# Kernel tuning notes

Hardware: AMD Instinct MI355X
Metric: run time of the kernel (lower is better)

## Reference

```python
import jax, jax.numpy as jnp
import numpy as np

N_INP = 256
N_OUT = 16
H = 1024
UH = 32  # uni_hidden_unit
BATCH = 16384


def setup_inputs() -> dict:
    key = jax.random.key(0)
    ks = jax.random.split(key, 16)
    s = 0.02
    return {
        "x": jax.random.normal(ks[0], (BATCH, N_INP), dtype=jnp.float32),
        # main MLP: n_inp -> 1024 -> 1024 -> n_out
        "W0": jax.random.normal(ks[1], (N_INP, H), dtype=jnp.float32) * s,
        "b0": jnp.zeros((H,), jnp.float32),
        "W1": jax.random.normal(ks[2], (H, H), dtype=jnp.float32) * s,
        "b1": jnp.zeros((H,), jnp.float32),
        "W2": jax.random.normal(ks[3], (H, N_OUT), dtype=jnp.float32) * s,
        "b2": jnp.zeros((N_OUT,), jnp.float32),
        # stacked per-feature uni MLPs: 1 -> UH -> UH -> n_out, one per feature
        "uw1": jax.random.normal(ks[4], (N_INP, UH), dtype=jnp.float32) * s,
        "ub1": jnp.zeros((N_INP, UH), jnp.float32),
        "uw2": jax.random.normal(ks[5], (N_INP, UH, UH), dtype=jnp.float32) * s,
        "ub2": jnp.zeros((N_INP, UH), jnp.float32),
        "uw3": jax.random.normal(ks[6], (N_INP, UH, N_OUT), dtype=jnp.float32) * s,
        "ub3": jnp.zeros((N_INP, N_OUT), jnp.float32),
    }


def reference(x, W0, b0, W1, b1, W2, b2, uw1, ub1, uw2, ub2, uw3, ub3):
    # main MLP: Linear+ReLU, Linear+ReLU, Linear
    y = jax.nn.relu(x @ W0 + b0)
    y = jax.nn.relu(y @ W1 + b1)
    y = y @ W2 + b2  # [B, n_out]

    # per-feature univariate MLPs, vectorized over the feature axis i
    # input to uni MLP i is x[:, i:i+1]  -> first Linear(1, UH)
    h = jax.nn.relu(x[:, :, None] * uw1[None] + ub1[None])       # [B, I, UH]
    h = jax.nn.relu(jnp.einsum('bif,ifo->bio', h, uw2) + ub2[None])  # [B, I, UH]
    u = jnp.einsum('bif,ifo->bio', h, uw3) + ub3[None]           # [B, I, n_out]
    return y + u.sum(axis=1)
```

## Files before the change

kernel.cpp:

```cpp
#include <hip/hip_runtime.h>

typedef unsigned short u16;
typedef __attribute__((ext_vector_type(4))) float f32x4;
typedef __attribute__((ext_vector_type(4))) int i32x4;
typedef __attribute__((ext_vector_type(8))) __bf16 bf16x8;
typedef __attribute__((ext_vector_type(4))) unsigned short u16x4;

#define BATCH 16384
#define NINP 256
#define HID 1024
#define NOUT 16

__device__ __forceinline__ u16 f2bf(float f) {
  unsigned u = __builtin_bit_cast(unsigned, f);
  u += 0x7FFFu + ((u >> 16) & 1u);
  return (u16)(u >> 16);
}
__device__ __forceinline__ f32x4 mfma_bb(bf16x8 a, bf16x8 b, f32x4 c) {
  return __builtin_amdgcn_mfma_f32_16x16x32_bf16(a, b, c, 0, 0, 0);
}
__device__ __forceinline__ void gload_lds16(const void* g, void* l) {
  __builtin_amdgcn_global_load_lds(
      (const __attribute__((address_space(1))) void*)g,
      (__attribute__((address_space(3))) void*)l, 16, 0, 0);
}

static const size_t OFF_H0    = 0;
static const size_t OFF_PARTU = 0;
static const size_t OFF_XB    = 33554432;
static const size_t OFF_PARTF = 33554432;
static const size_t OFF_W0T   = 67108864;
static const size_t OFF_W1T   = 67633152;
static const size_t OFF_W2T   = 69730304;
static const size_t OFF_UWP   = 69763072;
static const size_t OFF_CB    = 70811648;

__global__ __launch_bounds__(256) void k_prep(
    const float* __restrict__ x,
    const float* __restrict__ W0, const float* __restrict__ W1,
    const float* __restrict__ W2,
    const float* __restrict__ uw1, const float* __restrict__ ub1,
    const float* __restrict__ uw2, const float* __restrict__ ub2,
    const float* __restrict__ uw3, const float* __restrict__ b2,
    const float* __restrict__ ub3,
    u16* __restrict__ xb,
    u16* __restrict__ W0T, u16* __restrict__ W1T, u16* __restrict__ W2T,
    char* __restrict__ uwp, float* __restrict__ cb)
{
  __shared__ float tile[32][33];
  const int bid = blockIdx.x;
  const int tid = threadIdx.x;

  if (bid < 1312) {
    const float* src; u16* dst; int K, N, kb, ob;
    if (bid < 256)       { src = W0; dst = W0T; K = 256;  N = 1024; int t = bid;        kb = (t & 7) * 32;  ob = (t >> 3) * 32; }
    else if (bid < 1280) { src = W1; dst = W1T; K = 1024; N = 1024; int t = bid - 256;  kb = (t & 31) * 32; ob = (t >> 5) * 32; }
    else                 { src = W2; dst = W2T; K = 1024; N = 16;   int t = bid - 1280; kb = t * 32;        ob = 0; }
    const int tx = tid & 31, ty = tid >> 5;
    for (int r = ty; r < 32; r += 8)
      if (ob + tx < N) tile[r][tx] = src[(size_t)(kb + r) * N + ob + tx];
    __syncthreads();
    for (int r = ty; r < 32; r += 8)
      if (ob + r < N) dst[(size_t)(ob + r) * K + kb + tx] = f2bf(tile[tx][r]);
  } else if (bid < 5408) {
    const int idx = ((bid - 1312) * 256 + tid) * 4;
    const float4 v = *(const float4*)&x[idx];
    u16x4 o4 = { f2bf(v.x), f2bf(v.y), f2bf(v.z), f2bf(v.w) };
    *(u16x4*)&xb[idx] = o4;
  } else if (bid < 5664) {
    const int e = ((bid - 5408) * 256 + tid) * 4;
    const float4 v = *(const float4*)&uw2[e];
    const int i = e >> 10, f = (e >> 5) & 31, o = e & 31;
    const float vv[4] = { v.x, v.y, v.z, v.w };
    u16* blob16 = (u16*)(uwp + (size_t)i * 4096);
#pragma unroll
    for (int d = 0; d < 4; ++d) {
      const int oo = o + d;
      const int lane = ((f >> 3) << 4) | (oo & 15);
      blob16[256 + (oo >> 4) * 512 + lane * 8 + (f & 7)] = f2bf(vv[d]);
    }
  } else if (bid < 5792) {
    const int e = ((bid - 5664) * 256 + tid) * 4;
    const float4 v = *(const float4*)&uw3[e];
    const int i = e >> 9, f = (e >> 4) & 31, o2 = e & 15;
    const int s = (f < 16) ? (((f >> 2) << 3) + (f & 3))
                           : ((((f - 16) >> 2) << 3) + 4 + (f & 3));
    const float vv[4] = { v.x, v.y, v.z, v.w };
    u16* blob16 = (u16*)(uwp + (size_t)i * 4096);
#pragma unroll
    for (int d = 0; d < 4; ++d)
      blob16[1280 + ((s >> 3) * 16 + o2 + d) * 8 + (s & 7)] = f2bf(vv[d]);
  } else if (bid < 5816) {
    const int e4 = (bid - 5792) * 256 + tid;
    const int i = e4 / 24, r4 = e4 % 24;
    const float* src = (r4 < 8)  ? &uw1[i * 32 + r4 * 4]
                     : (r4 < 16) ? &ub1[i * 32 + (r4 - 8) * 4]
                                 : &ub2[i * 32 + (r4 - 16) * 4];
    *(float4*)(uwp + (size_t)i * 4096 + r4 * 16) = *(const float4*)src;
  } else {
    __shared__ float red[16][16];
    const int ig = tid >> 4, o = tid & 15;
    float s = 0.f;
#pragma unroll
    for (int k = 0; k < 16; ++k) s += ub3[(ig * 16 + k) * 16 + o];
    red[ig][o] = s;
    __syncthreads();
    if (tid < 16) {
      float t = b2[tid];
#pragma unroll
      for (int k = 0; k < 16; ++k) t += red[k][tid];
      cb[tid] = t;
    }
  }
}

template<int KT, bool FOLD>
__device__ __forceinline__ void gemm_body(
    const u16* __restrict__ A, const u16* __restrict__ BT,
    const float* __restrict__ bias, u16* __restrict__ C,
    const u16* __restrict__ W2Tp, float* __restrict__ pfold, int N)
{
  extern __shared__ __align__(16) char lds[];
  const int tid = threadIdx.x;
  const int lane = tid & 63, wid = tid >> 6;
  const int l15 = lane & 15, g = lane >> 4;
  const int wA = wid >> 2;
  const int wn = wid & 3;
  const int nbn = N >> 8;
  int logical = blockIdx.x;
  { const int nwg = gridDim.x;
    if ((nwg & 7) == 0) { const int q = nwg >> 3; logical = (logical & 7) * q + (logical >> 3); } }
  const int bm = logical / nbn, bn = logical - bm * nbn;
  const size_t rb = (size_t)bm * 256, cb = (size_t)bn * 256;

  const int q7 = l15 & 7;
  const int arow0 = wA * 128 + l15;
  const int brow0 = wn * 64 + l15;

  char* const ldsA = lds;
  char* const ldsB = lds + 65536;

  const u16* Ag = A + rb * KT;
  const u16* Bg = BT + cb * KT;

  bf16x8 w2f[8];
  if constexpr (FOLD) {
#pragma unroll
    for (int c = 0; c < 8; ++c)
      w2f[c] = __builtin_bit_cast(bf16x8,
          *(const i32x4*)&W2Tp[l15 * HID + (int)cb + c * 32 + g * 8]);
  }
  float bv[4];
#pragma unroll
  for (int n = 0; n < 4; ++n) bv[n] = bias[cb + wn * 64 + n * 16 + l15];

  f32x4 acc[8][4] = {};
  const int NT = KT >> 6;

#define STAGE(arr, src, ktE, s) do { \
    const int G_ = (s) * 512 + tid; \
    const int row_ = G_ >> 3; \
    const int c8_ = (G_ & 7) ^ (row_ & 7); \
    gload_lds16(&(src)[(size_t)row_ * KT + (ktE) + c8_ * 8], (arr) + G_ * 16); \
  } while (0)

#define ARD(bp, m, kk) (*(const bf16x8*)((bp) + (((arow0 + (m) * 16) * 8 + (((kk) * 4 + g) ^ q7)) << 4)))
#define BRD(bp, n, kk) (*(const bf16x8*)((bp) + (((brow0 + (n) * 16) * 8 + (((kk) * 4 + g) ^ q7)) << 4)))

#define KTILE(Ab, Bb, An, Bn, kt1, LASTT) do {                                 \
    bf16x8 av[4][2], bv0[2][2], bv1[2][2];                                     \
              \
    if (!(LASTT)) { STAGE(Bn, Bg, kt1, 0); STAGE(Bn, Bg, kt1, 1);              \
                    STAGE(Bn, Bg, kt1, 2); STAGE(Bn, Bg, kt1, 3);              \
                    STAGE(An, Ag, kt1, 0); STAGE(An, Ag, kt1, 2);              \
                    STAGE(An, Ag, kt1, 1); STAGE(An, Ag, kt1, 3); }            \
    _Pragma("unroll")                                                          \
    for (int m = 0; m < 4; ++m) { av[m][0] = ARD(Ab, m, 0); av[m][1] = ARD(Ab, m, 1); } \
    _Pragma("unroll")                                                          \
    for (int n = 0; n < 2; ++n) { bv0[n][0] = BRD(Bb, n, 0); bv0[n][1] = BRD(Bb, n, 1); \
                                  bv1[n][0] = BRD(Bb, n + 2, 0); bv1[n][1] = BRD(Bb, n + 2, 1); } \
    _Pragma("unroll")                                                          \
    for (int m = 0; m < 4; ++m)                                                \
      _Pragma("unroll")                                                        \
      for (int n = 0; n < 2; ++n) {                                            \
        acc[m][n]     = mfma_bb(av[m][0], bv0[n][0], acc[m][n]);               \
        acc[m][n]     = mfma_bb(av[m][1], bv0[n][1], acc[m][n]);               \
        acc[m][n + 2] = mfma_bb(av[m][0], bv1[n][0], acc[m][n + 2]);           \
        acc[m][n + 2] = mfma_bb(av[m][1], bv1[n][1], acc[m][n + 2]);           \
      }                                                                        \
    if (LASTT) { asm volatile("s_waitcnt vmcnt(0)" ::: "memory"); }            \
    else       { asm volatile("s_waitcnt vmcnt(8)" ::: "memory"); }            \
    asm volatile("s_barrier" ::: "memory");                                    \
                                             \
    _Pragma("unroll")                                                          \
    for (int m = 0; m < 4; ++m) { av[m][0] = ARD(Ab, m + 4, 0); av[m][1] = ARD(Ab, m + 4, 1); } \
    _Pragma("unroll")                                                          \
    for (int m = 0; m < 4; ++m)                                                \
      _Pragma("unroll")                                                        \
      for (int n = 0; n < 2; ++n) {                                            \
        acc[m + 4][n]     = mfma_bb(av[m][0], bv0[n][0], acc[m + 4][n]);       \
        acc[m + 4][n]     = mfma_bb(av[m][1], bv0[n][1], acc[m + 4][n]);       \
        acc[m + 4][n + 2] = mfma_bb(av[m][0], bv1[n][0], acc[m + 4][n + 2]);   \
        acc[m + 4][n + 2] = mfma_bb(av[m][1], bv1[n][1], acc[m + 4][n + 2]);   \
      }                                                                        \
    if (!(LASTT)) { asm volatile("s_waitcnt vmcnt(2)" ::: "memory"); }         \
    asm volatile("s_barrier" ::: "memory");                                    \
  } while (0)

  STAGE(ldsB, Bg, 0, 0); STAGE(ldsB, Bg, 0, 1);
  STAGE(ldsB, Bg, 0, 2); STAGE(ldsB, Bg, 0, 3);
  STAGE(ldsA, Ag, 0, 0); STAGE(ldsA, Ag, 0, 2);
  STAGE(ldsA, Ag, 0, 1); STAGE(ldsA, Ag, 0, 3);
  asm volatile("s_waitcnt vmcnt(2)" ::: "memory");
  asm volatile("s_barrier" ::: "memory");

  for (int t = 0; t < NT - 1; ++t) {
    const int b = t & 1;
    KTILE(ldsA + b * 32768, ldsB + b * 32768,
          ldsA + (b ^ 1) * 32768, ldsB + (b ^ 1) * 32768,
          (t + 1) << 6, false);
  }
  {
    const int b = (NT - 1) & 1;
    KTILE(ldsA + b * 32768, ldsB + b * 32768,
          ldsA + (b ^ 1) * 32768, ldsB + (b ^ 1) * 32768, 0, true);
  }
#undef KTILE
#undef STAGE
#undef ARD
#undef BRD

  asm volatile("s_waitcnt vmcnt(0)" ::: "memory");

  {
    char* const ep = lds;
#pragma unroll
    for (int h = 0; h < 2; ++h) {
      __syncthreads();
#pragma unroll
      for (int mloc = 0; mloc < 4; ++mloc)
#pragma unroll
        for (int n = 0; n < 4; ++n) {
          const int col = wn * 64 + n * 16 + l15;
#pragma unroll
          for (int r = 0; r < 4; ++r) {
            const int lrow = wA * 64 + mloc * 16 + g * 4 + r;
            *(u16*)(ep + lrow * 512 + ((col * 2) ^ ((lrow & 7) << 4))) =
                f2bf(fmaxf(acc[h * 4 + mloc][n][r] + bv[n], 0.f));
          }
        }
      __syncthreads();
      if constexpr (!FOLD) {
#pragma unroll
        for (int p = 0; p < 8; ++p) {
          const int ci = p * 512 + tid;
          const int lrow = ci >> 5, c16 = ci & 31;
          const i32x4 v = *(const i32x4*)(ep + lrow * 512 + ((c16 * 16) ^ ((lrow & 7) << 4)));
          const int grow = (int)rb + (lrow >> 6) * 128 + h * 64 + (lrow & 63);
          *(i32x4*)&C[(size_t)grow * N + cb + c16 * 8] = v;
        }
      } else {
        const int lrow = wid * 16 + l15;
        f32x4 accf = {0.f, 0.f, 0.f, 0.f};
#pragma unroll
        for (int c = 0; c < 8; ++c) {
          const bf16x8 afr = *(const bf16x8*)(
              ep + lrow * 512 + ((c * 64 + g * 16) ^ ((lrow & 7) << 4)));
          accf = mfma_bb(afr, w2f[c], accf);
        }
        const int rowb2 = (int)rb + (wid >> 2) * 128 + h * 64 + (wid & 3) * 16;
        float* pf = pfold + ((size_t)bn * BATCH + rowb2) * NOUT;
#pragma unroll
        for (int r = 0; r < 4; ++r)
          pf[(g * 4 + r) * NOUT + l15] = accf[r];
      }
    }
  }
}

__global__ __launch_bounds__(512, 2) void k_g1(
    const u16* __restrict__ A, const u16* __restrict__ BT,
    const float* __restrict__ bias, u16* __restrict__ C, int N)
{
  gemm_body<256, false>(A, BT, bias, C, nullptr, nullptr, N);
}
__global__ __launch_bounds__(512, 2) void k_g2(
    const u16* __restrict__ A, const u16* __restrict__ BT,
    const float* __restrict__ bias, const u16* __restrict__ W2Tp,
    float* __restrict__ pfold, int N)
{
  gemm_body<1024, true>(A, BT, bias, nullptr, W2Tp, pfold, N);
}

__global__ __launch_bounds__(256, 4) void k_uni(
    const float* __restrict__ x,
    const char* __restrict__ uwp,
    float* __restrict__ part)
{
  const int tid = threadIdx.x, lane = tid & 63, wid = tid >> 6;
  const int l15 = lane & 15, g = lane >> 4;
  const int chunk = blockIdx.x & 7, rowblk = blockIdx.x >> 3;
  const int rb_blk = rowblk * 128;
  const int rb = rb_blk + wid * 32;
  const int i0 = chunk * 32;

  __shared__ __align__(16) float xt[128][33];
  __shared__ __align__(16) char wbuf[3][4096];

  {
    const int r0 = tid >> 3, c4 = (tid & 7) << 2;
#pragma unroll
    for (int rr = 0; rr < 128; rr += 32)
      *(float4*)&xt[rr + r0][c4] =
          *(const float4*)&x[(size_t)(rb_blk + rr + r0) * NINP + i0 + c4];
  }
  gload_lds16(uwp + (size_t)i0 * 4096 + tid * 16, &wbuf[0][tid * 16]);
  gload_lds16(uwp + (size_t)(i0 + 1) * 4096 + tid * 16, &wbuf[1][tid * 16]);
  __syncthreads();

  const f32x4 zero4 = {0.f, 0.f, 0.f, 0.f};
  f32x4 acc0 = zero4, acc1 = zero4;
  const float* xr0 = &xt[wid * 32 + l15][0];
  const float* xr1 = &xt[wid * 32 + 16 + l15][0];

#pragma unroll 2
  for (int ii = 0; ii < 32; ++ii) {
    const int nf = i0 + ((ii + 2) & 31);
    gload_lds16(uwp + (size_t)nf * 4096 + tid * 16,
                &wbuf[(ii + 2) % 3][tid * 16]);

    const char* bp = &wbuf[ii % 3][0];
    const f32x4 w1lo = *(const f32x4*)(bp + g * 32);
    const f32x4 w1hi = *(const f32x4*)(bp + g * 32 + 16);
    const f32x4 b1lo = *(const f32x4*)(bp + 128 + g * 32);
    const f32x4 b1hi = *(const f32x4*)(bp + 128 + g * 32 + 16);
    const f32x4 bb0  = *(const f32x4*)(bp + 256 + g * 16);
    const f32x4 bb1  = *(const f32x4*)(bp + 320 + g * 16);
    const bf16x8 bv0 = *(const bf16x8*)(bp + 512 + lane * 16);
    const bf16x8 bv1 = *(const bf16x8*)(bp + 1536 + lane * 16);
    const bf16x8 b3  = *(const bf16x8*)(bp + 2560 + lane * 16);
    const float xv0 = xr0[ii], xv1 = xr1[ii];

    bf16x8 af0, af1;
#pragma unroll
    for (int j = 0; j < 4; ++j) {
      af0[j]     = (__bf16)fmaxf(fmaf(xv0, w1lo[j], b1lo[j]), 0.f);
      af0[4 + j] = (__bf16)fmaxf(fmaf(xv0, w1hi[j], b1hi[j]), 0.f);
      af1[j]     = (__bf16)fmaxf(fmaf(xv1, w1lo[j], b1lo[j]), 0.f);
      af1[4 + j] = (__bf16)fmaxf(fmaf(xv1, w1hi[j], b1hi[j]), 0.f);
    }

    const f32x4 d00 = mfma_bb(bv0, af0, bb0);
    const f32x4 d10 = mfma_bb(bv1, af0, bb1);
    const f32x4 d01 = mfma_bb(bv0, af1, bb0);
    const f32x4 d11 = mfma_bb(bv1, af1, bb1);

    bf16x8 h20, h21;
#pragma unroll
    for (int j = 0; j < 4; ++j) {
      h20[j]     = (__bf16)fmaxf(d00[j], 0.f);
      h20[4 + j] = (__bf16)fmaxf(d10[j], 0.f);
      h21[j]     = (__bf16)fmaxf(d01[j], 0.f);
      h21[4 + j] = (__bf16)fmaxf(d11[j], 0.f);
    }

    acc0 = mfma_bb(b3, h20, acc0);
    acc1 = mfma_bb(b3, h21, acc1);

    asm volatile("s_waitcnt vmcnt(1)" ::: "memory");
    __builtin_amdgcn_s_barrier();
  }

  float* p = part + ((size_t)chunk * BATCH + rb) * NOUT;
  *(f32x4*)&p[l15 * 16 + g * 4] = acc0;
  *(f32x4*)&p[(16 + l15) * 16 + g * 4] = acc1;
}

__global__ __launch_bounds__(256) void k_reduce(
    const float* __restrict__ pu, const float* __restrict__ pf,
    const float* __restrict__ cb, float* __restrict__ out)
{
  const int j4 = blockIdx.x * 256 + threadIdx.x;
  const float4 c = ((const float4*)cb)[j4 & 3];
  const float4* a4 = (const float4*)pu;
  const float4* b4 = (const float4*)pf;
  float rx = c.x, ry = c.y, rz = c.z, rw = c.w;
#pragma unroll
  for (int cc = 0; cc < 8; ++cc) {
    const float4 a = a4[cc * 65536 + j4];
    rx += a.x; ry += a.y; rz += a.z; rw += a.w;
  }
#pragma unroll
  for (int cc = 0; cc < 4; ++cc) {
    const float4 a = b4[cc * 65536 + j4];
    rx += a.x; ry += a.y; rz += a.z; rw += a.w;
  }
  float4 r; r.x = rx; r.y = ry; r.z = rz; r.w = rw;
  ((float4*)out)[j4] = r;
}

extern "C" void kernel_launch(void* const* d_in, const int* in_sizes, int n_in,
                              void* d_out, int out_size, void* d_ws, size_t ws_size,
                              hipStream_t stream) {
  (void)in_sizes; (void)n_in; (void)out_size; (void)ws_size;
  const float* x   = (const float*)d_in[0];
  const float* W0  = (const float*)d_in[1];
  const float* b0  = (const float*)d_in[2];
  const float* W1  = (const float*)d_in[3];
  const float* b1  = (const float*)d_in[4];
  const float* W2  = (const float*)d_in[5];
  const float* b2  = (const float*)d_in[6];
  const float* uw1 = (const float*)d_in[7];
  const float* ub1 = (const float*)d_in[8];
  const float* uw2 = (const float*)d_in[9];
  const float* ub2 = (const float*)d_in[10];
  const float* uw3 = (const float*)d_in[11];
  const float* ub3 = (const float*)d_in[12];
  float* out = (float*)d_out;

  char* ws = (char*)d_ws;
  u16*   H0    = (u16*)(ws + OFF_H0);
  u16*   xb    = (u16*)(ws + OFF_XB);
  u16*   W0T   = (u16*)(ws + OFF_W0T);
  u16*   W1T   = (u16*)(ws + OFF_W1T);
  u16*   W2T   = (u16*)(ws + OFF_W2T);
  char*  uwp   = (char*)(ws + OFF_UWP);
  float* cb    = (float*)(ws + OFF_CB);
  float* partu = (float*)(ws + OFF_PARTU);
  float* partf = (float*)(ws + OFF_PARTF);

  hipFuncSetAttribute((const void*)k_g1,
                      hipFuncAttributeMaxDynamicSharedMemorySize, 131072);
  hipFuncSetAttribute((const void*)k_g2,
                      hipFuncAttributeMaxDynamicSharedMemorySize, 131072);

  k_prep<<<5817, 256, 0, stream>>>(x, W0, W1, W2, uw1, ub1, uw2, ub2, uw3,
                                   b2, ub3, xb, W0T, W1T, W2T, uwp, cb);
  k_g1<<<256, 512, 131072, stream>>>(xb, W0T, b0, H0, HID);
  k_g2<<<256, 512, 131072, stream>>>(H0, W1T, b1, W2T, partf, HID);
  k_uni<<<1024, 256, 0, stream>>>(x, uwp, partu);
  k_reduce<<<256, 256, 0, stream>>>(partu, partf, cb, out);
}
```

Baseline: 97.71 us.

## Use 4-wave 128x128 warp tiles with 8x8 MFMA accumulators in GEMMs

Restructures the two MLP GEMM kernels from 8 waves per 256x256 tile to 4 waves, each owning a 128x128 sub-tile with an 8x8 accumulator grid. The aim is fewer LDS fragment reads per MFMA, which raises arithmetic intensity per wave. The k-tile loop is simplified to issue all prefetches, load every fragment, and run the MFMAs under raised s_setprio, with a full vmcnt(0) wait per tile. The cost is much higher register pressure (256 accumulator floats per lane), lower occupancy at one 256-thread block, and less overlap between loads and compute inside a tile.

```diff
diff --git a/kernel.cpp b/kernel.cpp
--- a/kernel.cpp
+++ b/kernel.cpp
@@ -124,8 +124,8 @@
   const int tid = threadIdx.x;
   const int lane = tid & 63, wid = tid >> 6;
   const int l15 = lane & 15, g = lane >> 4;
-  const int wA = wid >> 2;
-  const int wn = wid & 3;
+  const int wA = wid >> 1;
+  const int wB = wid & 1;
   const int nbn = N >> 8;
   int logical = blockIdx.x;
   { const int nwg = gridDim.x;
@@ -135,7 +135,7 @@
 
   const int q7 = l15 & 7;
   const int arow0 = wA * 128 + l15;
-  const int brow0 = wn * 64 + l15;
+  const int brow0 = wB * 128 + l15;
 
   char* const ldsA = lds;
   char* const ldsB = lds + 65536;
@@ -150,15 +150,15 @@
       w2f[c] = __builtin_bit_cast(bf16x8,
           *(const i32x4*)&W2Tp[l15 * HID + (int)cb + c * 32 + g * 8]);
   }
-  float bv[4];
-#pragma unroll
-  for (int n = 0; n < 4; ++n) bv[n] = bias[cb + wn * 64 + n * 16 + l15];
-
-  f32x4 acc[8][4] = {};
+  float bvs[8];
+#pragma unroll
+  for (int n = 0; n < 8; ++n) bvs[n] = bias[cb + wB * 128 + n * 16 + l15];
+
+  f32x4 acc[8][8] = {};
   const int NT = KT >> 6;
 
 #define STAGE(arr, src, ktE, s) do { \
-    const int G_ = (s) * 512 + tid; \
+    const int G_ = (s) * 256 + tid; \
     const int row_ = G_ >> 3; \
     const int c8_ = (G_ & 7) ^ (row_ & 7); \
     gload_lds16(&(src)[(size_t)row_ * KT + (ktE) + c8_ * 8], (arr) + G_ * 16); \
@@ -168,50 +168,42 @@
 #define BRD(bp, n, kk) (*(const bf16x8*)((bp) + (((brow0 + (n) * 16) * 8 + (((kk) * 4 + g) ^ q7)) << 4)))
 
 #define KTILE(Ab, Bb, An, Bn, kt1, LASTT) do {                                 \
-    bf16x8 av[4][2], bv0[2][2], bv1[2][2];                                     \
-              \
-    if (!(LASTT)) { STAGE(Bn, Bg, kt1, 0); STAGE(Bn, Bg, kt1, 1);              \
-                    STAGE(Bn, Bg, kt1, 2); STAGE(Bn, Bg, kt1, 3);              \
-                    STAGE(An, Ag, kt1, 0); STAGE(An, Ag, kt1, 2);              \
-                    STAGE(An, Ag, kt1, 1); STAGE(An, Ag, kt1, 3); }            \
-    _Pragma("unroll")                                                          \
-    for (int m = 0; m < 4; ++m) { av[m][0] = ARD(Ab, m, 0); av[m][1] = ARD(Ab, m, 1); } \
-    _Pragma("unroll")                                                          \
-    for (int n = 0; n < 2; ++n) { bv0[n][0] = BRD(Bb, n, 0); bv0[n][1] = BRD(Bb, n, 1); \
-                                  bv1[n][0] = BRD(Bb, n + 2, 0); bv1[n][1] = BRD(Bb, n + 2, 1); } \
-    _Pragma("unroll")                                                          \
-    for (int m = 0; m < 4; ++m)                                                \
+    if (!(LASTT)) {                                                            \
       _Pragma("unroll")                                                        \
-      for (int n = 0; n < 2; ++n) {                                            \
-        acc[m][n]     = mfma_bb(av[m][0], bv0[n][0], acc[m][n]);               \
-        acc[m][n]     = mfma_bb(av[m][1], bv0[n][1], acc[m][n]);               \
-        acc[m][n + 2] = mfma_bb(av[m][0], bv1[n][0], acc[m][n + 2]);           \
-        acc[m][n + 2] = mfma_bb(av[m][1], bv1[n][1], acc[m][n + 2]);           \
-      }                                                                        \
-    if (LASTT) { asm volatile("s_waitcnt vmcnt(0)" ::: "memory"); }            \
-    else       { asm volatile("s_waitcnt vmcnt(8)" ::: "memory"); }            \
-    asm volatile("s_barrier" ::: "memory");                                    \
-                                             \
-    _Pragma("unroll")                                                          \
-    for (int m = 0; m < 4; ++m) { av[m][0] = ARD(Ab, m + 4, 0); av[m][1] = ARD(Ab, m + 4, 1); } \
-    _Pragma("unroll")                                                          \
-    for (int m = 0; m < 4; ++m)                                                \
+      for (int s = 0; s < 8; ++s) STAGE(An, Ag, kt1, s);                       \
       _Pragma("unroll")                                                        \
-      for (int n = 0; n < 2; ++n) {                                            \
-        acc[m + 4][n]     = mfma_bb(av[m][0], bv0[n][0], acc[m + 4][n]);       \
-        acc[m + 4][n]     = mfma_bb(av[m][1], bv0[n][1], acc[m + 4][n]);       \
-        acc[m + 4][n + 2] = mfma_bb(av[m][0], bv1[n][0], acc[m + 4][n + 2]);   \
-        acc[m + 4][n + 2] = mfma_bb(av[m][1], bv1[n][1], acc[m + 4][n + 2]);   \
-      }                                                                        \
-    if (!(LASTT)) { asm volatile("s_waitcnt vmcnt(2)" ::: "memory"); }         \
+      for (int s = 0; s < 8; ++s) STAGE(Bn, Bg, kt1, s);                       \
+    }                                                                          \
+    bf16x8 a0[8], b0[8], a1[8], b1[8];                                         \
+    _Pragma("unroll")                                                          \
+    for (int m = 0; m < 8; ++m) a0[m] = ARD(Ab, m, 0);                         \
+    _Pragma("unroll")                                                          \
+    for (int n = 0; n < 8; ++n) b0[n] = BRD(Bb, n, 0);                         \
+    _Pragma("unroll")                                                          \
+    for (int m = 0; m < 8; ++m) a1[m] = ARD(Ab, m, 1);                         \
+    _Pragma("unroll")                                                          \
+    for (int n = 0; n < 8; ++n) b1[n] = BRD(Bb, n, 1);                         \
+    __builtin_amdgcn_s_setprio(1);                                             \
+    _Pragma("unroll")                                                          \
+    for (int m = 0; m < 8; ++m)                                                \
+      _Pragma("unroll")                                                        \
+      for (int n = 0; n < 8; ++n)                                              \
+        acc[m][n] = mfma_bb(a0[m], b0[n], acc[m][n]);                          \
+    _Pragma("unroll")                                                          \
+    for (int m = 0; m < 8; ++m)                                                \
+      _Pragma("unroll")                                                        \
+      for (int n = 0; n < 8; ++n)                                              \
+        acc[m][n] = mfma_bb(a1[m], b1[n], acc[m][n]);                          \
+    __builtin_amdgcn_s_setprio(0);                                             \
+    asm volatile("s_waitcnt vmcnt(0)" ::: "memory");                           \
     asm volatile("s_barrier" ::: "memory");                                    \
   } while (0)
 
-  STAGE(ldsB, Bg, 0, 0); STAGE(ldsB, Bg, 0, 1);
-  STAGE(ldsB, Bg, 0, 2); STAGE(ldsB, Bg, 0, 3);
-  STAGE(ldsA, Ag, 0, 0); STAGE(ldsA, Ag, 0, 2);
-  STAGE(ldsA, Ag, 0, 1); STAGE(ldsA, Ag, 0, 3);
-  asm volatile("s_waitcnt vmcnt(2)" ::: "memory");
+#pragma unroll
+  for (int s = 0; s < 8; ++s) STAGE(ldsA, Ag, 0, s);
+#pragma unroll
+  for (int s = 0; s < 8; ++s) STAGE(ldsB, Bg, 0, s);
+  asm volatile("s_waitcnt vmcnt(0)" ::: "memory");
   asm volatile("s_barrier" ::: "memory");
 
   for (int t = 0; t < NT - 1; ++t) {
@@ -230,8 +222,6 @@
 #undef ARD
 #undef BRD
 
-  asm volatile("s_waitcnt vmcnt(0)" ::: "memory");
-
   {
     char* const ep = lds;
 #pragma unroll
@@ -240,51 +230,55 @@
 #pragma unroll
       for (int mloc = 0; mloc < 4; ++mloc)
 #pragma unroll
-        for (int n = 0; n < 4; ++n) {
-          const int col = wn * 64 + n * 16 + l15;
+        for (int n = 0; n < 8; ++n) {
+          const int col = wB * 128 + n * 16 + l15;
 #pragma unroll
           for (int r = 0; r < 4; ++r) {
             const int lrow = wA * 64 + mloc * 16 + g * 4 + r;
             *(u16*)(ep + lrow * 512 + ((col * 2) ^ ((lrow & 7) << 4))) =
-                f2bf(fmaxf(acc[h * 4 + mloc][n][r] + bv[n], 0.f));
+                f2bf(fmaxf(acc[h * 4 + mloc][n][r] + bvs[n], 0.f));
           }
         }
       __syncthreads();
       if constexpr (!FOLD) {
 #pragma unroll
-        for (int p = 0; p < 8; ++p) {
-          const int ci = p * 512 + tid;
+        for (int p = 0; p < 16; ++p) {
+          const int ci = p * 256 + tid;
           const int lrow = ci >> 5, c16 = ci & 31;
           const i32x4 v = *(const i32x4*)(ep + lrow * 512 + ((c16 * 16) ^ ((lrow & 7) << 4)));
           const int grow = (int)rb + (lrow >> 6) * 128 + h * 64 + (lrow & 63);
           *(i32x4*)&C[(size_t)grow * N + cb + c16 * 8] = v;
         }
       } else {
-        const int lrow = wid * 16 + l15;
-        f32x4 accf = {0.f, 0.f, 0.f, 0.f};
-#pragma unroll
-        for (int c = 0; c < 8; ++c) {
-          const bf16x8 afr = *(const bf16x8*)(
-              ep + lrow * 512 + ((c * 64 + g * 16) ^ ((lrow & 7) << 4)));
-          accf = mfma_bb(afr, w2f[c], accf);
+#pragma unroll
+        for (int s = 0; s < 2; ++s) {
+          const int lrow = wid * 32 + s * 16 + l15;
+          f32x4 accf = {0.f, 0.f, 0.f, 0.f};
+#pragma unroll
+          for (int c = 0; c < 8; ++c) {
+            const bf16x8 afr = *(const bf16x8*)(
+                ep + lrow * 512 + ((c * 64 + g * 16) ^ ((lrow & 7) << 4)));
+            accf = mfma_bb(afr, w2f[c], accf);
+          }
+          const int rowb2 = (int)rb + (wid >> 1) * 128 + h * 64 +
+                            (wid & 1) * 32 + s * 16;
+          float* pf = pfold + ((size_t)bn * BATCH + rowb2) * NOUT;
+#pragma unroll
+          for (int r = 0; r < 4; ++r)
+            pf[(g * 4 + r) * NOUT + l15] = accf[r];
         }
-        const int rowb2 = (int)rb + (wid >> 2) * 128 + h * 64 + (wid & 3) * 16;
-        float* pf = pfold + ((size_t)bn * BATCH + rowb2) * NOUT;
-#pragma unroll
-        for (int r = 0; r < 4; ++r)
-          pf[(g * 4 + r) * NOUT + l15] = accf[r];
       }
     }
   }
 }
 
-__global__ __launch_bounds__(512, 2) void k_g1(
+__global__ __launch_bounds__(256, 1) void k_g1(
     const u16* __restrict__ A, const u16* __restrict__ BT,
     const float* __restrict__ bias, u16* __restrict__ C, int N)
 {
   gemm_body<256, false>(A, BT, bias, C, nullptr, nullptr, N);
 }
-__global__ __launch_bounds__(512, 2) void k_g2(
+__global__ __launch_bounds__(256, 1) void k_g2(
     const u16* __restrict__ A, const u16* __restrict__ BT,
     const float* __restrict__ bias, const u16* __restrict__ W2Tp,
     float* __restrict__ pfold, int N)
@@ -436,8 +430,8 @@
 
   k_prep<<<5817, 256, 0, stream>>>(x, W0, W1, W2, uw1, ub1, uw2, ub2, uw3,
                                    b2, ub3, xb, W0T, W1T, W2T, uwp, cb);
-  k_g1<<<256, 512, 131072, stream>>>(xb, W0T, b0, H0, HID);
-  k_g2<<<256, 512, 131072, stream>>>(H0, W1T, b1, W2T, partf, HID);
+  k_g1<<<256, 256, 131072, stream>>>(xb, W0T, b0, H0, HID);
+  k_g2<<<256, 256, 131072, stream>>>(H0, W1T, b1, W2T, partf, HID);
   k_uni<<<1024, 256, 0, stream>>>(x, uwp, partu);
   k_reduce<<<256, 256, 0, stream>>>(partu, partf, cb, out);
 }
```

New measurement: 100.9 us. 1.03x slower.
